# Kernel optimization log

Hardware: AMD Instinct MI355X
Metric: run time of the kernel (lower is better)

Reference implementation:

```python
import jax, jax.numpy as jnp
import numpy as np


def setup_inputs() -> dict:
    key = jax.random.key(0)
    ks = jax.random.split(key, 8)
    C = 256
    Cq = C // 8  # 32
    B, H, W = 4, 64, 64
    x = jax.random.normal(ks[0], (B, C, H, W), dtype=jnp.float32)
    wq = jax.random.normal(ks[1], (Cq, C), dtype=jnp.float32) * (1.0 / np.sqrt(C))
    bq = jax.random.normal(ks[2], (Cq,), dtype=jnp.float32) * 0.01
    wk = jax.random.normal(ks[3], (Cq, C), dtype=jnp.float32) * (1.0 / np.sqrt(C))
    bk = jax.random.normal(ks[4], (Cq,), dtype=jnp.float32) * 0.01
    wv = jax.random.normal(ks[5], (C, C), dtype=jnp.float32) * (1.0 / np.sqrt(C))
    bv = jax.random.normal(ks[6], (C,), dtype=jnp.float32) * 0.01
    gamma = jax.random.normal(ks[7], (1,), dtype=jnp.float32)
    return {"x": x, "wq": wq, "bq": bq, "wk": wk, "bk": bk,
            "wv": wv, "bv": bv, "gamma": gamma}


def reference(x, wq, bq, wk, bk, wv, bv, gamma):
    B, C, H, W = x.shape
    N = H * W
    xf = x.reshape(B, C, N)  # [B, C, N] flattened spatial
    # 1x1 convs == per-position linear projections
    q = jnp.einsum('oc,bcn->bno', wq, xf) + bq          # [B, N, Cq]
    k = jnp.einsum('oc,bcn->bon', wk, xf) + bk[:, None]  # [B, Cq, N]
    v = jnp.einsum('oc,bcn->bon', wv, xf) + bv[:, None]  # [B, C, N]
    attn = jax.nn.softmax(jnp.einsum('bnc,bcm->bnm', q, k), axis=-1)  # [B, N, N]
    # out[b,c,n] = sum_m v[b,c,m] * attn[n,m]
    out = jnp.einsum('bcm,bnm->bcn', v, attn).reshape(B, C, H, W)
    return gamma[0] * out + x
```

## Files before the change

kernel.cpp:

```cpp
#include <hip/hip_runtime.h>

#define BB 4
#define CC 256
#define CQ 32
#define NN 4096

#define QT_OFF 0
#define KT_OFF (BB*NN*CQ)
#define VT_OFF (2*BB*NN*CQ)
#define WB_OFF (VT_OFF + BB*CC*NN)
#define BIAS_OFF (WB_OFF + 320*256)

#define LDS_BARRIER() asm volatile("s_waitcnt lgkmcnt(0)\ns_barrier" ::: "memory")

typedef __attribute__((ext_vector_type(8))) short bf16x8;
typedef __attribute__((ext_vector_type(4))) short bf16x4;
typedef __attribute__((ext_vector_type(4))) float f32x4;

__device__ inline unsigned short f2bf(float f) {
    unsigned int u = __float_as_uint(f);
    u += 0x7fffu + ((u >> 16) & 1u);
    return (unsigned short)(u >> 16);
}

__global__ __launch_bounds__(256) void prepw_kernel(
    const float* __restrict__ wq, const float* __restrict__ bq,
    const float* __restrict__ wk, const float* __restrict__ bk,
    const float* __restrict__ wv, const float* __restrict__ bv,
    unsigned short* __restrict__ ws)
{
    unsigned short* Wb = ws + WB_OFF;
    float* Bias = (float*)(ws + BIAS_OFF);
    int idx = blockIdx.x * 256 + threadIdx.x;
    if (idx < 320 * 256) {
        int row = idx >> 8, col = idx & 255;
        float v = row < 32 ? wq[row * 256 + col]
                : row < 64 ? wk[(row - 32) * 256 + col]
                           : wv[(row - 64) * 256 + col];
        Wb[idx] = f2bf(v);
    }
    if (idx < 320)
        Bias[idx] = idx < 32 ? bq[idx] : idx < 64 ? bk[idx - 32] : bv[idx - 64];
}

__global__ __launch_bounds__(256, 2) void qkv_kernel(
    const float* __restrict__ x, unsigned short* __restrict__ ws)
{
    __shared__ __align__(16) unsigned short xs[32][264];
    __shared__ __align__(16) unsigned short vs[256][40];
    const int t = threadIdx.x;
    const int w = t >> 6, l = t & 63, quad = l >> 4, lc = l & 15;
    const int b = blockIdx.y, n0 = blockIdx.x * 32;

    unsigned short* qT = ws + QT_OFF;
    unsigned short* kT = ws + KT_OFF;
    const unsigned short* Wb = ws + WB_OFF;
    const float* Bias = (const float*)(ws + BIAS_OFF);

    const float* xb = x + (size_t)(b * CC) * NN + n0;
    {
        const int nq = t & 7, swz = (nq & 3) << 3;
#pragma unroll
        for (int u = 0; u < 2; ++u) {
            const int c0 = (t >> 3) * 4 + u * 128;
            f32x4 r0 = *(const f32x4*)&xb[(size_t)(c0 + 0) * NN + nq * 4];
            f32x4 r1 = *(const f32x4*)&xb[(size_t)(c0 + 1) * NN + nq * 4];
            f32x4 r2 = *(const f32x4*)&xb[(size_t)(c0 + 2) * NN + nq * 4];
            f32x4 r3 = *(const f32x4*)&xb[(size_t)(c0 + 3) * NN + nq * 4];
            const int cs = c0 ^ swz;
#pragma unroll
            for (int k = 0; k < 4; ++k) {
                bf16x4 w4;
                w4[0] = (short)f2bf(r0[k]);
                w4[1] = (short)f2bf(r1[k]);
                w4[2] = (short)f2bf(r2[k]);
                w4[3] = (short)f2bf(r3[k]);
                *(bf16x4*)&xs[nq * 4 + k][cs] = w4;
            }
        }
    }
    __syncthreads();

    f32x4 acc[5][2];
#pragma unroll
    for (int j = 0; j < 5; ++j) {
        f32x4 b4 = *(const f32x4*)&Bias[(w * 5 + j) * 16 + quad * 4];
        acc[j][0] = b4; acc[j][1] = b4;
    }

#pragma unroll
    for (int s = 0; s < 8; ++s) {
        bf16x8 Af[5], Bf[2];
#pragma unroll
        for (int j = 0; j < 5; ++j)
            Af[j] = *(const bf16x8*)&Wb[((w * 5 + j) * 16 + lc) * 256 + s * 32 + quad * 8];
#pragma unroll
        for (int nt = 0; nt < 2; ++nt) {
            int pos = nt * 16 + lc;
            int col = (s * 32 + quad * 8) ^ (((pos >> 2) & 3) << 3);
            Bf[nt] = *(const bf16x8*)&xs[pos][col];
        }
#pragma unroll
        for (int j = 0; j < 5; ++j)
#pragma unroll
            for (int nt = 0; nt < 2; ++nt)
                acc[j][nt] = __builtin_amdgcn_mfma_f32_16x16x32_bf16(Af[j], Bf[nt], acc[j][nt], 0, 0, 0);
    }

#pragma unroll
    for (int j = 0; j < 5; ++j) {
        int ot = w * 5 + j;
#pragma unroll
        for (int nt = 0; nt < 2; ++nt) {
            if (ot < 4) {
                bf16x4 pk;
#pragma unroll
                for (int i = 0; i < 4; ++i) pk[i] = (short)f2bf(acc[j][nt][i]);
                unsigned short* bas = (ot < 2 ? qT : kT);
                int ocl = (ot & 1) * 16 + quad * 4;
                *(bf16x4*)&bas[((size_t)(b * NN + n0 + nt * 16 + lc)) * CQ + ocl] = pk;
            } else {
#pragma unroll
                for (int i = 0; i < 4; ++i)
                    vs[(ot - 4) * 16 + quad * 4 + i][nt * 16 + lc] = f2bf(acc[j][nt][i]);
            }
        }
    }
    __syncthreads();

    const int mt = n0 >> 6, hb = (n0 >> 5) & 1;
    unsigned short* vt = ws + VT_OFF + ((size_t)(b * 64 + mt) * 16) * 1024 + hb * 512;
#pragma unroll
    for (int p = 0; p < 4; ++p) {
        int ci = p * 256 + t;
        int ct = ci >> 6, g = (ci >> 4) & 3, lcp = ci & 15;
        bf16x8 chunk = *(const bf16x8*)&vs[ct * 16 + lcp][g * 8];
        *(bf16x8*)&vt[(size_t)ct * 1024 + g * 128 + lcp * 8] = chunk;
    }
}

__global__ __launch_bounds__(1024, 4) void attn_kernel(
    const float* __restrict__ x, const unsigned short* __restrict__ ws,
    const float* __restrict__ gamma, float* __restrict__ out)
{
    __shared__ __align__(16) unsigned short Ps[2][4][4][512];
    __shared__ __align__(16) float lSpart[2][64];

    const int t = threadIdx.x;
    const int w = t >> 6, l = t & 63, quad = l >> 4, lc = l & 15;
    const int id = blockIdx.x, xcd = id & 7;
    const int b = xcd >> 1;
    const int n0 = (((id >> 3) << 1) | (xcd & 1)) * 64;
    const int role = (w + (w >> 2)) & 1;
    const int r = (w >> 2) * 2 + ((w & 3) >> 1);

    const unsigned short* qT = ws + QT_OFF;
    const unsigned short* kb = ws + KT_OFF + (size_t)b * NN * CQ;
    const unsigned short* vbase = ws + VT_OFF + ((size_t)b << 20);

    if (role == 0) {
        const int qg = r & 3, kh = r >> 2;
        const bf16x8 bqf =
            *(const bf16x8*)&qT[((size_t)(b * NN + n0 + qg * 16 + lc)) * CQ + quad * 8];
        const f32x4 z = {0.f, 0.f, 0.f, 0.f};

        bf16x8 kA[4], kB[4];
        auto loadK = [&](bf16x8* kr, int tt) {
            int m0 = (tt & 31) * 128 + kh * 64;
#pragma unroll
            for (int j = 0; j < 4; ++j)
                kr[j] = *(const bf16x8*)&kb[(size_t)(m0 + j * 16 + lc) * CQ + quad * 8];
        };

        f32x4 sn[4];
        float lacc = 0.f;

        auto expj = [&](int pp, int j) {
            bf16x4 pk;
#pragma unroll
            for (int i = 0; i < 4; ++i) {
                float p = __expf(sn[j][i]);
                lacc += p;
                pk[i] = (short)f2bf(p);
            }
            int ks = kh * 2 + (j >> 1);
            int lanep = ((2 * j + (quad >> 1)) & 3) * 16 + lc;
            *(bf16x4*)&Ps[pp][qg][ks][lanep * 8 + (quad & 1) * 4] = pk;
        };

        auto qkbody = [&](int tt, bf16x8* kUse, bf16x8* kNext) {
#pragma unroll
            for (int j = 0; j < 4; ++j)
                sn[j] = __builtin_amdgcn_mfma_f32_16x16x32_bf16(kUse[j], bqf, z, 0, 0, 0);
            loadK(kNext, tt + 2);
#pragma unroll
            for (int j = 0; j < 4; ++j) expj((tt + 1) & 1, j);
            LDS_BARRIER();
        };

        loadK(kA, 0);
#pragma unroll
        for (int j = 0; j < 4; ++j)
            sn[j] = __builtin_amdgcn_mfma_f32_16x16x32_bf16(kA[j], bqf, z, 0, 0, 0);
        loadK(kA, 1);
#pragma unroll
        for (int j = 0; j < 4; ++j) expj(0, j);
        LDS_BARRIER();

        for (int it = 0; it < 15; ++it) {
            qkbody(2 * it,     kA, kB);
            qkbody(2 * it + 1, kB, kA);
        }
        qkbody(30, kA, kB);

        lacc += __shfl_xor(lacc, 16);
        lacc += __shfl_xor(lacc, 32);
        if (quad == 0) lSpart[kh][qg * 16 + lc] = lacc;
        LDS_BARRIER();
    } else {
        const int rv = r;

        f32x4 acc[4][2];
#pragma unroll
        for (int i = 0; i < 4; ++i)
#pragma unroll
            for (int j = 0; j < 2; ++j) acc[i][j] = (f32x4){0.f, 0.f, 0.f, 0.f};

        bf16x8 va[2][2], vb2[2][2];
        auto loadVhalf = [&](bf16x8 (*vr)[2], int tt, int half) {
            int m = (tt & 31) * 2 + half;
#pragma unroll
            for (int c = 0; c < 2; ++c) {
                int ct = rv * 2 + c;
#pragma unroll
                for (int kk = 0; kk < 2; ++kk)
                    vr[c][kk] = *(const bf16x8*)&vbase[((size_t)m * 16 + ct) * 1024 + kk * 512 + l * 8];
            }
        };

        auto pvks = [&](int pp, int ks, const bf16x8& v0, const bf16x8& v1) {
            bf16x8 ap[4];
#pragma unroll
            for (int qs = 0; qs < 4; ++qs)
                ap[qs] = *(const bf16x8*)&Ps[pp][qs][ks][l * 8];
            __builtin_amdgcn_s_setprio(1);
#pragma unroll
            for (int qs = 0; qs < 4; ++qs) {
                acc[qs][0] = __builtin_amdgcn_mfma_f32_16x16x32_bf16(ap[qs], v0, acc[qs][0], 0, 0, 0);
                acc[qs][1] = __builtin_amdgcn_mfma_f32_16x16x32_bf16(ap[qs], v1, acc[qs][1], 0, 0, 0);
            }
            __builtin_amdgcn_s_setprio(0);
        };

        loadVhalf(va, 0, 0);
        loadVhalf(vb2, 0, 1);
        LDS_BARRIER();

        for (int tt = 0; tt < 31; ++tt) {
            int pp = tt & 1;
            pvks(pp, 0, va[0][0], va[1][0]);
            pvks(pp, 1, va[0][1], va[1][1]);
            loadVhalf(va, tt + 1, 0);
            pvks(pp, 2, vb2[0][0], vb2[1][0]);
            pvks(pp, 3, vb2[0][1], vb2[1][1]);
            loadVhalf(vb2, tt + 1, 1);
            LDS_BARRIER();
        }
        pvks(1, 0, va[0][0], va[1][0]);
        pvks(1, 1, va[0][1], va[1][1]);
        pvks(1, 2, vb2[0][0], vb2[1][0]);
        pvks(1, 3, vb2[0][1], vb2[1][1]);
        LDS_BARRIER();

        const float g = gamma[0];
#pragma unroll
        for (int qs = 0; qs < 4; ++qs) {
            f32x4 l0 = *(const f32x4*)&lSpart[0][qs * 16 + quad * 4];
            f32x4 l1 = *(const f32x4*)&lSpart[1][qs * 16 + quad * 4];
            f32x4 rl;
#pragma unroll
            for (int i = 0; i < 4; ++i) rl[i] = 1.f / (l0[i] + l1[i]);
#pragma unroll
            for (int c2 = 0; c2 < 2; ++c2) {
                int c = rv * 32 + c2 * 16 + lc;
                size_t base = ((size_t)(b * CC + c)) * NN + n0 + qs * 16 + quad * 4;
                f32x4 xr = *(const f32x4*)&x[base];
                f32x4 o;
#pragma unroll
                for (int i = 0; i < 4; ++i) o[i] = g * acc[qs][c2][i] * rl[i] + xr[i];
                *(f32x4*)&out[base] = o;
            }
        }
    }
}

extern "C" void kernel_launch(void* const* d_in, const int* in_sizes, int n_in,
                              void* d_out, int out_size, void* d_ws, size_t ws_size,
                              hipStream_t stream) {
    const float* x     = (const float*)d_in[0];
    const float* wq    = (const float*)d_in[1];
    const float* bq    = (const float*)d_in[2];
    const float* wk    = (const float*)d_in[3];
    const float* bk    = (const float*)d_in[4];
    const float* wv    = (const float*)d_in[5];
    const float* bv    = (const float*)d_in[6];
    const float* gamma = (const float*)d_in[7];
    float* out = (float*)d_out;
    unsigned short* ws = (unsigned short*)d_ws;

    prepw_kernel<<<320, 256, 0, stream>>>(wq, bq, wk, bk, wv, bv, ws);
    dim3 g1(NN / 32, BB);
    qkv_kernel<<<g1, 256, 0, stream>>>(x, ws);
    attn_kernel<<<256, 1024, 0, stream>>>(x, ws, gamma, out);
}
```

Before: 136.7 us.

## Quad-buffer P tiles to halve barriers and software-pipeline LDS reads in PV

The shared P buffer grows from two to four stages, so the QK producer waves compute two K tiles per barrier and the barrier count is halved. The PV consumer waves double-buffer their LDS fragment loads (apA/apB), fetching the next k-slice while MFMAs run on the current one, and prefetch the next tile's first slice across the barrier boundary. The goal is to cut barrier stalls and hide LDS latency behind MFMA work. The cost is twice the LDS for P, which may lower occupancy, plus more live registers.

Measured after the change: 142.4 us. 1.04x slower.

```diff
diff --git a/kernel.cpp b/kernel.cpp
--- a/kernel.cpp
+++ b/kernel.cpp
@@ -143,7 +143,7 @@
     const float* __restrict__ x, const unsigned short* __restrict__ ws,
     const float* __restrict__ gamma, float* __restrict__ out)
 {
-    __shared__ __align__(16) unsigned short Ps[2][4][4][512];
+    __shared__ __align__(16) unsigned short Ps[4][4][4][512];
     __shared__ __align__(16) float lSpart[2][64];
 
     const int t = threadIdx.x;
@@ -188,30 +188,26 @@
             *(bf16x4*)&Ps[pp][qg][ks][lanep * 8 + (quad & 1) * 4] = pk;
         };
 
-        auto qkbody = [&](int tt, bf16x8* kUse, bf16x8* kNext) {
+        auto qkstep = [&](int tt, bf16x8* kUse) {
 #pragma unroll
             for (int j = 0; j < 4; ++j)
                 sn[j] = __builtin_amdgcn_mfma_f32_16x16x32_bf16(kUse[j], bqf, z, 0, 0, 0);
-            loadK(kNext, tt + 2);
-#pragma unroll
-            for (int j = 0; j < 4; ++j) expj((tt + 1) & 1, j);
+            loadK(kUse, tt + 2);
+#pragma unroll
+            for (int j = 0; j < 4; ++j) expj(tt & 3, j);
+        };
+
+        loadK(kA, 0);
+        loadK(kB, 1);
+        qkstep(0, kA);
+        qkstep(1, kB);
+        LDS_BARRIER();
+
+        for (int s = 0; s < 15; ++s) {
+            qkstep(2 * s + 2, kA);
+            qkstep(2 * s + 3, kB);
             LDS_BARRIER();
-        };
-
-        loadK(kA, 0);
-#pragma unroll
-        for (int j = 0; j < 4; ++j)
-            sn[j] = __builtin_amdgcn_mfma_f32_16x16x32_bf16(kA[j], bqf, z, 0, 0, 0);
-        loadK(kA, 1);
-#pragma unroll
-        for (int j = 0; j < 4; ++j) expj(0, j);
-        LDS_BARRIER();
-
-        for (int it = 0; it < 15; ++it) {
-            qkbody(2 * it,     kA, kB);
-            qkbody(2 * it + 1, kB, kA);
-        }
-        qkbody(30, kA, kB);
+        }
 
         lacc += __shfl_xor(lacc, 16);
         lacc += __shfl_xor(lacc, 32);
@@ -238,11 +234,14 @@
             }
         };
 
-        auto pvks = [&](int pp, int ks, const bf16x8& v0, const bf16x8& v1) {
-            bf16x8 ap[4];
+        bf16x8 apA[4], apB[4];
+        auto loadAp = [&](bf16x8* dst, int pp, int ks) {
 #pragma unroll
             for (int qs = 0; qs < 4; ++qs)
-                ap[qs] = *(const bf16x8*)&Ps[pp][qs][ks][l * 8];
+                dst[qs] = *(const bf16x8*)&Ps[pp][qs][ks][l * 8];
+        };
+
+        auto mfmaCluster = [&](const bf16x8* ap, const bf16x8& v0, const bf16x8& v1) {
             __builtin_amdgcn_s_setprio(1);
 #pragma unroll
             for (int qs = 0; qs < 4; ++qs) {
@@ -252,24 +251,33 @@
             __builtin_amdgcn_s_setprio(0);
         };
 
+        auto pvtile = [&](int tt, int pfTile) {
+            int pp = tt & 3;
+            loadAp(apB, pp, 1);
+            mfmaCluster(apA, va[0][0], va[1][0]);
+            loadAp(apA, pp, 2);
+            mfmaCluster(apB, va[0][1], va[1][1]);
+            loadVhalf(va, tt + 1, 0);
+            loadAp(apB, pp, 3);
+            mfmaCluster(apA, vb2[0][0], vb2[1][0]);
+            if (pfTile >= 0) loadAp(apA, pfTile & 3, 0);
+            mfmaCluster(apB, vb2[0][1], vb2[1][1]);
+            loadVhalf(vb2, tt + 1, 1);
+        };
+
         loadVhalf(va, 0, 0);
         loadVhalf(vb2, 0, 1);
         LDS_BARRIER();
-
-        for (int tt = 0; tt < 31; ++tt) {
-            int pp = tt & 1;
-            pvks(pp, 0, va[0][0], va[1][0]);
-            pvks(pp, 1, va[0][1], va[1][1]);
-            loadVhalf(va, tt + 1, 0);
-            pvks(pp, 2, vb2[0][0], vb2[1][0]);
-            pvks(pp, 3, vb2[0][1], vb2[1][1]);
-            loadVhalf(vb2, tt + 1, 1);
+        loadAp(apA, 0, 0);
+
+        for (int s = 0; s < 15; ++s) {
+            pvtile(2 * s,     2 * s + 1);
+            pvtile(2 * s + 1, -1);
             LDS_BARRIER();
-        }
-        pvks(1, 0, va[0][0], va[1][0]);
-        pvks(1, 1, va[0][1], va[1][1]);
-        pvks(1, 2, vb2[0][0], vb2[1][0]);
-        pvks(1, 3, vb2[0][1], vb2[1][1]);
+            loadAp(apA, (2 * s + 2) & 3, 0);
+        }
+        pvtile(30, 31);
+        pvtile(31, -1);
         LDS_BARRIER();
 
         const float g = gamma[0];
```

## Split PV accumulation over key halves across waves and reduce through LDS

Applied to the files above, without the earlier changes.

Each PV wave now owns 64 output channels, up from 32, and handles only one half of each key tile. This halves the reloads of P fragments from LDS per wave and raises MFMA work per P load. The two partial sums are combined through a new 64KB LDS scratch buffer at the end. The QK waves get an extra barrier to stay in step. The cost is twice the accumulator registers, more LDS use that may limit occupancy, and an extra reduction step.

Result: no change. 137.6 us (+0.6%).

```diff
diff --git a/kernel.cpp b/kernel.cpp
--- a/kernel.cpp
+++ b/kernel.cpp
@@ -145,6 +145,7 @@
 {
     __shared__ __align__(16) unsigned short Ps[2][4][4][512];
     __shared__ __align__(16) float lSpart[2][64];
+    __shared__ __align__(16) float scr[4 * 16 * 64 * 4];
 
     const int t = threadIdx.x;
     const int w = t >> 6, l = t & 63, quad = l >> 4, lc = l & 15;
@@ -217,78 +218,84 @@
         lacc += __shfl_xor(lacc, 32);
         if (quad == 0) lSpart[kh][qg * 16 + lc] = lacc;
         LDS_BARRIER();
+        LDS_BARRIER();
     } else {
-        const int rv = r;
-
-        f32x4 acc[4][2];
+        const int p = r >> 1, ksh = r & 1;
+
+        f32x4 acc[4][4];
 #pragma unroll
         for (int i = 0; i < 4; ++i)
 #pragma unroll
-            for (int j = 0; j < 2; ++j) acc[i][j] = (f32x4){0.f, 0.f, 0.f, 0.f};
-
-        bf16x8 va[2][2], vb2[2][2];
-        auto loadVhalf = [&](bf16x8 (*vr)[2], int tt, int half) {
-            int m = (tt & 31) * 2 + half;
-#pragma unroll
-            for (int c = 0; c < 2; ++c) {
-                int ct = rv * 2 + c;
-#pragma unroll
-                for (int kk = 0; kk < 2; ++kk)
-                    vr[c][kk] = *(const bf16x8*)&vbase[((size_t)m * 16 + ct) * 1024 + kk * 512 + l * 8];
-            }
-        };
-
-        auto pvks = [&](int pp, int ks, const bf16x8& v0, const bf16x8& v1) {
-            bf16x8 ap[4];
+            for (int j = 0; j < 4; ++j) acc[i][j] = (f32x4){0.f, 0.f, 0.f, 0.f};
+
+        bf16x8 vf[4][2];
+        auto loadVkk = [&](int tt, int kk) {
+            int m = (tt & 31) * 2 + ksh;
+#pragma unroll
+            for (int c = 0; c < 4; ++c) {
+                int ct = p * 4 + c;
+                vf[c][kk] = *(const bf16x8*)&vbase[((size_t)m * 16 + ct) * 1024 + kk * 512 + l * 8];
+            }
+        };
+
+        auto pvtile = [&](int pp, int tt) {
+#pragma unroll
+            for (int kk = 0; kk < 2; ++kk) {
+                bf16x8 ap[4];
+#pragma unroll
+                for (int qs = 0; qs < 4; ++qs)
+                    ap[qs] = *(const bf16x8*)&Ps[pp][qs][2 * ksh + kk][l * 8];
+                __builtin_amdgcn_s_setprio(1);
+#pragma unroll
+                for (int qs = 0; qs < 4; ++qs)
+#pragma unroll
+                    for (int c = 0; c < 4; ++c)
+                        acc[qs][c] = __builtin_amdgcn_mfma_f32_16x16x32_bf16(ap[qs], vf[c][kk], acc[qs][c], 0, 0, 0);
+                __builtin_amdgcn_s_setprio(0);
+                loadVkk(tt + 1, kk);
+            }
+        };
+
+        loadVkk(0, 0);
+        loadVkk(0, 1);
+        LDS_BARRIER();
+
+        for (int tt = 0; tt < 31; ++tt) {
+            pvtile(tt & 1, tt);
+            LDS_BARRIER();
+        }
+        pvtile(1, 31);
+        LDS_BARRIER();
+
+        if (ksh == 0) {
 #pragma unroll
             for (int qs = 0; qs < 4; ++qs)
-                ap[qs] = *(const bf16x8*)&Ps[pp][qs][ks][l * 8];
-            __builtin_amdgcn_s_setprio(1);
+#pragma unroll
+                for (int c = 0; c < 4; ++c)
+                    *(f32x4*)&scr[((p * 16 + qs * 4 + c) * 64 + l) * 4] = acc[qs][c];
+        }
+        LDS_BARRIER();
+        if (ksh == 1) {
+            const float g = gamma[0];
 #pragma unroll
             for (int qs = 0; qs < 4; ++qs) {
-                acc[qs][0] = __builtin_amdgcn_mfma_f32_16x16x32_bf16(ap[qs], v0, acc[qs][0], 0, 0, 0);
-                acc[qs][1] = __builtin_amdgcn_mfma_f32_16x16x32_bf16(ap[qs], v1, acc[qs][1], 0, 0, 0);
-            }
-            __builtin_amdgcn_s_setprio(0);
-        };
-
-        loadVhalf(va, 0, 0);
-        loadVhalf(vb2, 0, 1);
-        LDS_BARRIER();
-
-        for (int tt = 0; tt < 31; ++tt) {
-            int pp = tt & 1;
-            pvks(pp, 0, va[0][0], va[1][0]);
-            pvks(pp, 1, va[0][1], va[1][1]);
-            loadVhalf(va, tt + 1, 0);
-            pvks(pp, 2, vb2[0][0], vb2[1][0]);
-            pvks(pp, 3, vb2[0][1], vb2[1][1]);
-            loadVhalf(vb2, tt + 1, 1);
-            LDS_BARRIER();
-        }
-        pvks(1, 0, va[0][0], va[1][0]);
-        pvks(1, 1, va[0][1], va[1][1]);
-        pvks(1, 2, vb2[0][0], vb2[1][0]);
-        pvks(1, 3, vb2[0][1], vb2[1][1]);
-        LDS_BARRIER();
-
-        const float g = gamma[0];
-#pragma unroll
-        for (int qs = 0; qs < 4; ++qs) {
-            f32x4 l0 = *(const f32x4*)&lSpart[0][qs * 16 + quad * 4];
-            f32x4 l1 = *(const f32x4*)&lSpart[1][qs * 16 + quad * 4];
-            f32x4 rl;
-#pragma unroll
-            for (int i = 0; i < 4; ++i) rl[i] = 1.f / (l0[i] + l1[i]);
-#pragma unroll
-            for (int c2 = 0; c2 < 2; ++c2) {
-                int c = rv * 32 + c2 * 16 + lc;
-                size_t base = ((size_t)(b * CC + c)) * NN + n0 + qs * 16 + quad * 4;
-                f32x4 xr = *(const f32x4*)&x[base];
-                f32x4 o;
-#pragma unroll
-                for (int i = 0; i < 4; ++i) o[i] = g * acc[qs][c2][i] * rl[i] + xr[i];
-                *(f32x4*)&out[base] = o;
+                f32x4 l0 = *(const f32x4*)&lSpart[0][qs * 16 + quad * 4];
+                f32x4 l1 = *(const f32x4*)&lSpart[1][qs * 16 + quad * 4];
+                f32x4 rl;
+#pragma unroll
+                for (int i = 0; i < 4; ++i) rl[i] = 1.f / (l0[i] + l1[i]);
+#pragma unroll
+                for (int c = 0; c < 4; ++c) {
+                    f32x4 oth = *(const f32x4*)&scr[((p * 16 + qs * 4 + c) * 64 + l) * 4];
+                    int ch = p * 64 + c * 16 + lc;
+                    size_t base = ((size_t)(b * CC + ch)) * NN + n0 + qs * 16 + quad * 4;
+                    f32x4 xr = *(const f32x4*)&x[base];
+                    f32x4 o;
+#pragma unroll
+                    for (int i = 0; i < 4; ++i)
+                        o[i] = g * (acc[qs][c][i] + oth[i]) * rl[i] + xr[i];
+                    *(f32x4*)&out[base] = o;
+                }
             }
         }
     }
```

## Fuse weight prep, QKV projection and attention into one cooperative kernel

Applied to the files above, without the earlier changes.

Merges the three launches (weight conversion, QKV projection, attention) into one cooperative kernel with 256 blocks of 1024 threads, using grid-wide syncs between phases. Each block now computes the QKV projection for 64 positions, matching its attention tile, and a single shared-memory buffer is reused across phases. The aim is to remove launch overheads and inter-kernel gaps. In exchange it adds two grid.sync barriers, requires all 256 blocks to be co-resident, and runs the projection phase at lower per-thread work with 1024-thread blocks.

Result: slower. 220.9 us (+61.5%).

```diff
diff --git a/kernel.cpp b/kernel.cpp
--- a/kernel.cpp
+++ b/kernel.cpp
@@ -1,4 +1,7 @@
 #include <hip/hip_runtime.h>
+#include <hip/hip_cooperative_groups.h>
+
+namespace cg = cooperative_groups;
 
 #define BB 4
 #define CC 256
@@ -23,46 +26,52 @@
     return (unsigned short)(u >> 16);
 }
 
-__global__ __launch_bounds__(256) void prepw_kernel(
+__global__ __launch_bounds__(1024, 4) void fused_kernel(
+    const float* __restrict__ x,
     const float* __restrict__ wq, const float* __restrict__ bq,
     const float* __restrict__ wk, const float* __restrict__ bk,
     const float* __restrict__ wv, const float* __restrict__ bv,
-    unsigned short* __restrict__ ws)
+    const float* __restrict__ gamma,
+    unsigned short* __restrict__ ws, float* __restrict__ out)
 {
+    __shared__ __align__(16) unsigned char smem[74752];
+
+    const int t = threadIdx.x;
+    const int w = t >> 6, l = t & 63, quad = l >> 4, lc = l & 15;
+    const int id = blockIdx.x, xcd = id & 7;
+    const int b = xcd >> 1;
+    const int n0 = (((id >> 3) << 1) | (xcd & 1)) * 64;
+
+    unsigned short* qT = ws + QT_OFF;
+    unsigned short* kT = ws + KT_OFF;
     unsigned short* Wb = ws + WB_OFF;
     float* Bias = (float*)(ws + BIAS_OFF);
-    int idx = blockIdx.x * 256 + threadIdx.x;
-    if (idx < 320 * 256) {
-        int row = idx >> 8, col = idx & 255;
-        float v = row < 32 ? wq[row * 256 + col]
-                : row < 64 ? wk[(row - 32) * 256 + col]
-                           : wv[(row - 64) * 256 + col];
-        Wb[idx] = f2bf(v);
+
+    cg::grid_group grid = cg::this_grid();
+
+    {
+        int idx = id * 1024 + t;
+        if (idx < 320 * 256) {
+            int row = idx >> 8, col = idx & 255;
+            float v = row < 32 ? wq[row * 256 + col]
+                    : row < 64 ? wk[(row - 32) * 256 + col]
+                               : wv[(row - 64) * 256 + col];
+            Wb[idx] = f2bf(v);
+        }
+        if (idx < 320)
+            Bias[idx] = idx < 32 ? bq[idx] : idx < 64 ? bk[idx - 32] : bv[idx - 64];
     }
-    if (idx < 320)
-        Bias[idx] = idx < 32 ? bq[idx] : idx < 64 ? bk[idx - 32] : bv[idx - 64];
-}
-
-__global__ __launch_bounds__(256, 2) void qkv_kernel(
-    const float* __restrict__ x, unsigned short* __restrict__ ws)
-{
-    __shared__ __align__(16) unsigned short xs[32][264];
-    __shared__ __align__(16) unsigned short vs[256][40];
-    const int t = threadIdx.x;
-    const int w = t >> 6, l = t & 63, quad = l >> 4, lc = l & 15;
-    const int b = blockIdx.y, n0 = blockIdx.x * 32;
-
-    unsigned short* qT = ws + QT_OFF;
-    unsigned short* kT = ws + KT_OFF;
-    const unsigned short* Wb = ws + WB_OFF;
-    const float* Bias = (const float*)(ws + BIAS_OFF);
-
-    const float* xb = x + (size_t)(b * CC) * NN + n0;
+    grid.sync();
+
     {
-        const int nq = t & 7, swz = (nq & 3) << 3;
-#pragma unroll
-        for (int u = 0; u < 2; ++u) {
-            const int c0 = (t >> 3) * 4 + u * 128;
+        auto xs = (unsigned short (*)[32][264])smem;
+        auto vs = (unsigned short (*)[256][40])(smem + 33792);
+
+        {
+            const int ti = t >> 9, tl = t & 511;
+            const int nq = tl & 7, swz = (nq & 3) << 3;
+            const int c0 = (tl >> 3) * 4;
+            const float* xb = x + (size_t)(b * CC) * NN + n0 + ti * 32;
             f32x4 r0 = *(const f32x4*)&xb[(size_t)(c0 + 0) * NN + nq * 4];
             f32x4 r1 = *(const f32x4*)&xb[(size_t)(c0 + 1) * NN + nq * 4];
             f32x4 r2 = *(const f32x4*)&xb[(size_t)(c0 + 2) * NN + nq * 4];
@@ -75,86 +84,73 @@
                 w4[1] = (short)f2bf(r1[k]);
                 w4[2] = (short)f2bf(r2[k]);
                 w4[3] = (short)f2bf(r3[k]);
-                *(bf16x4*)&xs[nq * 4 + k][cs] = w4;
+                *(bf16x4*)&xs[ti][nq * 4 + k][cs] = w4;
+            }
+        }
+        __syncthreads();
+
+        {
+            const int ti = w >> 3, g = w & 3, nt = (w >> 2) & 1;
+
+            f32x4 acc[5];
+#pragma unroll
+            for (int j = 0; j < 5; ++j)
+                acc[j] = *(const f32x4*)&Bias[(g * 5 + j) * 16 + quad * 4];
+
+#pragma unroll
+            for (int s = 0; s < 8; ++s) {
+                bf16x8 Af[5], Bf;
+#pragma unroll
+                for (int j = 0; j < 5; ++j)
+                    Af[j] = *(const bf16x8*)&Wb[((g * 5 + j) * 16 + lc) * 256 + s * 32 + quad * 8];
+                int pos = nt * 16 + lc;
+                int col = (s * 32 + quad * 8) ^ (((pos >> 2) & 3) << 3);
+                Bf = *(const bf16x8*)&xs[ti][pos][col];
+#pragma unroll
+                for (int j = 0; j < 5; ++j)
+                    acc[j] = __builtin_amdgcn_mfma_f32_16x16x32_bf16(Af[j], Bf, acc[j], 0, 0, 0);
+            }
+
+#pragma unroll
+            for (int j = 0; j < 5; ++j) {
+                int ot = g * 5 + j;
+                if (ot < 4) {
+                    bf16x4 pk;
+#pragma unroll
+                    for (int i = 0; i < 4; ++i) pk[i] = (short)f2bf(acc[j][i]);
+                    unsigned short* bas = (ot < 2 ? qT : kT);
+                    int ocl = (ot & 1) * 16 + quad * 4;
+                    *(bf16x4*)&bas[((size_t)(b * NN + n0 + ti * 32 + nt * 16 + lc)) * CQ + ocl] = pk;
+                } else {
+#pragma unroll
+                    for (int i = 0; i < 4; ++i)
+                        vs[ti][(ot - 4) * 16 + quad * 4 + i][nt * 16 + lc] = f2bf(acc[j][i]);
+                }
+            }
+        }
+        __syncthreads();
+
+        {
+            const int mt = n0 >> 6;
+#pragma unroll
+            for (int p = 0; p < 2; ++p) {
+                int ci = p * 1024 + t;
+                int ti2 = ci >> 10, cj = ci & 1023;
+                int ct = cj >> 6, g2 = (cj >> 4) & 3, lcp = cj & 15;
+                unsigned short* vt = ws + VT_OFF + ((size_t)(b * 64 + mt) * 16) * 1024 + ti2 * 512;
+                bf16x8 chunk = *(const bf16x8*)&vs[ti2][ct * 16 + lcp][g2 * 8];
+                *(bf16x8*)&vt[(size_t)ct * 1024 + g2 * 128 + lcp * 8] = chunk;
             }
         }
     }
-    __syncthreads();
-
-    f32x4 acc[5][2];
-#pragma unroll
-    for (int j = 0; j < 5; ++j) {
-        f32x4 b4 = *(const f32x4*)&Bias[(w * 5 + j) * 16 + quad * 4];
-        acc[j][0] = b4; acc[j][1] = b4;
-    }
-
-#pragma unroll
-    for (int s = 0; s < 8; ++s) {
-        bf16x8 Af[5], Bf[2];
-#pragma unroll
-        for (int j = 0; j < 5; ++j)
-            Af[j] = *(const bf16x8*)&Wb[((w * 5 + j) * 16 + lc) * 256 + s * 32 + quad * 8];
-#pragma unroll
-        for (int nt = 0; nt < 2; ++nt) {
-            int pos = nt * 16 + lc;
-            int col = (s * 32 + quad * 8) ^ (((pos >> 2) & 3) << 3);
-            Bf[nt] = *(const bf16x8*)&xs[pos][col];
-        }
-#pragma unroll
-        for (int j = 0; j < 5; ++j)
-#pragma unroll
-            for (int nt = 0; nt < 2; ++nt)
-                acc[j][nt] = __builtin_amdgcn_mfma_f32_16x16x32_bf16(Af[j], Bf[nt], acc[j][nt], 0, 0, 0);
-    }
-
-#pragma unroll
-    for (int j = 0; j < 5; ++j) {
-        int ot = w * 5 + j;
-#pragma unroll
-        for (int nt = 0; nt < 2; ++nt) {
-            if (ot < 4) {
-                bf16x4 pk;
-#pragma unroll
-                for (int i = 0; i < 4; ++i) pk[i] = (short)f2bf(acc[j][nt][i]);
-                unsigned short* bas = (ot < 2 ? qT : kT);
-                int ocl = (ot & 1) * 16 + quad * 4;
-                *(bf16x4*)&bas[((size_t)(b * NN + n0 + nt * 16 + lc)) * CQ + ocl] = pk;
-            } else {
-#pragma unroll
-                for (int i = 0; i < 4; ++i)
-                    vs[(ot - 4) * 16 + quad * 4 + i][nt * 16 + lc] = f2bf(acc[j][nt][i]);
-            }
-        }
-    }
-    __syncthreads();
-
-    const int mt = n0 >> 6, hb = (n0 >> 5) & 1;
-    unsigned short* vt = ws + VT_OFF + ((size_t)(b * 64 + mt) * 16) * 1024 + hb * 512;
-#pragma unroll
-    for (int p = 0; p < 4; ++p) {
-        int ci = p * 256 + t;
-        int ct = ci >> 6, g = (ci >> 4) & 3, lcp = ci & 15;
-        bf16x8 chunk = *(const bf16x8*)&vs[ct * 16 + lcp][g * 8];
-        *(bf16x8*)&vt[(size_t)ct * 1024 + g * 128 + lcp * 8] = chunk;
-    }
-}
-
-__global__ __launch_bounds__(1024, 4) void attn_kernel(
-    const float* __restrict__ x, const unsigned short* __restrict__ ws,
-    const float* __restrict__ gamma, float* __restrict__ out)
-{
-    __shared__ __align__(16) unsigned short Ps[2][4][4][512];
-    __shared__ __align__(16) float lSpart[2][64];
-
-    const int t = threadIdx.x;
-    const int w = t >> 6, l = t & 63, quad = l >> 4, lc = l & 15;
-    const int id = blockIdx.x, xcd = id & 7;
-    const int b = xcd >> 1;
-    const int n0 = (((id >> 3) << 1) | (xcd & 1)) * 64;
+    grid.sync();
+
+    auto Ps = (unsigned short (*)[4][4][512])smem;
+    auto lSpart = (float (*)[64])(smem + 32768);
+
     const int role = (w + (w >> 2)) & 1;
     const int r = (w >> 2) * 2 + ((w & 3) >> 1);
 
-    const unsigned short* qT = ws + QT_OFF;
     const unsigned short* kb = ws + KT_OFF + (size_t)b * NN * CQ;
     const unsigned short* vbase = ws + VT_OFF + ((size_t)b << 20);
 
@@ -308,8 +304,8 @@
     float* out = (float*)d_out;
     unsigned short* ws = (unsigned short*)d_ws;
 
-    prepw_kernel<<<320, 256, 0, stream>>>(wq, bq, wk, bk, wv, bv, ws);
-    dim3 g1(NN / 32, BB);
-    qkv_kernel<<<g1, 256, 0, stream>>>(x, ws);
-    attn_kernel<<<256, 1024, 0, stream>>>(x, ws, gamma, out);
+    void* args[] = { (void*)&x, (void*)&wq, (void*)&bq, (void*)&wk, (void*)&bk,
+                     (void*)&wv, (void*)&bv, (void*)&gamma, (void*)&ws, (void*)&out };
+    hipLaunchCooperativeKernel(reinterpret_cast<void*>(fused_kernel),
+                               dim3(256), dim3(1024), args, 0, stream);
 }
```
